# Optimization experiments

Measured on AMD Instinct MI355X. Metric: run time of the kernel, lower is better.

## Reference

```python
import jax, jax.numpy as jnp
import numpy as np

B, S, D, H = 4, 2048, 2048, 16
HD = D // H            # 128 head dim
HID = 5632             # SwiGLU hidden: multiple_of*ceil((2/3*4*D)/multiple_of)
EPS = 1e-6


def setup_inputs() -> dict:
    key = jax.random.key(0)
    ks = jax.random.split(key, 12)
    s = 0.02
    x = jax.random.normal(ks[0], (B, S, D), dtype=jnp.float32)
    # RoPE freqs (theta=10000), complex freqs_cis represented as cos/sin
    inv_freq = 1.0 / (10000.0 ** (np.arange(0, HD, 2, dtype=np.float32) / HD))
    t = np.arange(S, dtype=np.float32)
    ang = np.outer(t, inv_freq)                      # [S, HD/2]
    freqs_cos = jnp.asarray(np.cos(ang), dtype=jnp.float32)
    freqs_sin = jnp.asarray(np.sin(ang), dtype=jnp.float32)
    # additive causal mask [1,1,S,S]
    mask = jnp.where(jnp.triu(jnp.ones((S, S), dtype=bool), k=1), -jnp.inf, 0.0)
    mask = mask.astype(jnp.float32)[None, None]
    return {
        "x": x,
        "freqs_cos": freqs_cos,
        "freqs_sin": freqs_sin,
        "mask": mask,
        "wq": jax.random.normal(ks[1], (D, D), jnp.float32) * s,
        "wk": jax.random.normal(ks[2], (D, D), jnp.float32) * s,
        "wv": jax.random.normal(ks[3], (D, D), jnp.float32) * s,
        "wo": jax.random.normal(ks[4], (D, D), jnp.float32) * s,
        "w1": jax.random.normal(ks[5], (HID, D), jnp.float32) * s,
        "w2": jax.random.normal(ks[6], (D, HID), jnp.float32) * s,
        "w3": jax.random.normal(ks[7], (HID, D), jnp.float32) * s,
        "attn_norm_w": jnp.ones((D,), jnp.float32),
        "ffn_norm_w": jnp.ones((D,), jnp.float32),
        "start_pos": 0,
    }


def rmsnorm(x, w, eps=EPS):
    xf = x.astype(jnp.float32)
    y = xf * jax.lax.rsqrt(jnp.mean(xf * xf, axis=-1, keepdims=True) + eps)
    return y.astype(x.dtype) * w


def apply_rope(q, k, cos, sin):
    # q,k: [B,S,H,HD]; cos,sin: [S,HD/2]
    def rot(x):
        xf = x.astype(jnp.float32).reshape(*x.shape[:-1], HD // 2, 2)
        xr, xi = xf[..., 0], xf[..., 1]
        c = cos[None, :, None, :]
        s = sin[None, :, None, :]
        out = jnp.stack([xr * c - xi * s, xr * s + xi * c], axis=-1)
        return out.reshape(*x.shape).astype(x.dtype)
    return rot(q), rot(k)


def reference(x, freqs_cos, freqs_sin, mask, wq, wk, wv, wo, w1, w2, w3,
              attn_norm_w, ffn_norm_w, start_pos):
    # ---- attention ----
    xa = rmsnorm(x, attn_norm_w)
    q = (xa @ wq.T).reshape(B, S, H, HD)
    k = (xa @ wk.T).reshape(B, S, H, HD)
    v = (xa @ wv.T).reshape(B, S, H, HD)
    q, k = apply_rope(q, k, freqs_cos, freqs_sin)
    # [B,H,S,S] scores (naive, materialized as in original)
    scores = jnp.einsum('bqhd,bkhd->bhqk', q, k) / jnp.sqrt(jnp.float32(HD))
    scores = scores + mask
    attn = jax.nn.softmax(scores, axis=-1)
    o = jnp.einsum('bhqk,bkhd->bqhd', attn, v).reshape(B, S, D)
    h = x + o @ wo.T
    # ---- SwiGLU FFN ----
    hf = rmsnorm(h, ffn_norm_w)
    ff = (jax.nn.silu(hf @ w1.T) * (hf @ w3.T)) @ w2.T
    return h + ff
```

## Files before the change

kernel.cpp:

```cpp
#include <hip/hip_runtime.h>
#include <hip/hip_bf16.h>
#include <stdint.h>

typedef short  bf16x8_t __attribute__((ext_vector_type(8)));
typedef short  bf16x4_t __attribute__((ext_vector_type(4)));
typedef float  f32x4_t  __attribute__((ext_vector_type(4)));
typedef unsigned short u16;
typedef unsigned int   u32;

#define DEV __device__ __forceinline__

DEV u16 f2bf(float f){
  u32 u = __float_as_uint(f);
  u += 0x7fffu + ((u >> 16) & 1u);
  return (u16)(u >> 16);
}
DEV float bf2f(u16 h){ return __uint_as_float(((u32)h) << 16); }

DEV void gl16(const void* g, void* l){
  __builtin_amdgcn_global_load_lds(
      (const __attribute__((address_space(1))) void*)g,
      (__attribute__((address_space(3))) void*)l, 16, 0, 0);
}

#define BAR() __builtin_amdgcn_s_barrier()
#define WL8() asm volatile("s_waitcnt lgkmcnt(8)" ::: "memory")
#define WL0() asm volatile("s_waitcnt lgkmcnt(0)" ::: "memory")

__global__ __launch_bounds__(256) void cvt_k(const float* __restrict__ in,
                                             u16* __restrict__ out, int n8){
  int i = blockIdx.x * 256 + threadIdx.x;
  if (i >= n8) return;
  const float4* p = (const float4*)in;
  float4 a = p[(size_t)i*2], b = p[(size_t)i*2+1];
  bf16x8_t o;
  o[0]=(short)f2bf(a.x); o[1]=(short)f2bf(a.y); o[2]=(short)f2bf(a.z); o[3]=(short)f2bf(a.w);
  o[4]=(short)f2bf(b.x); o[5]=(short)f2bf(b.y); o[6]=(short)f2bf(b.z); o[7]=(short)f2bf(b.w);
  *(bf16x8_t*)(out + (size_t)i*8) = o;
}

__global__ __launch_bounds__(256) void rmsnorm_k(const float* __restrict__ x,
                                                 const float* __restrict__ w,
                                                 u16* __restrict__ y){
  int row = blockIdx.x, t = threadIdx.x;
  const float4* xr = (const float4*)(x + (size_t)row*2048);
  float4 a = xr[t*2], b = xr[t*2+1];
  float ss = a.x*a.x+a.y*a.y+a.z*a.z+a.w*a.w + b.x*b.x+b.y*b.y+b.z*b.z+b.w*b.w;
  #pragma unroll
  for (int m = 32; m; m >>= 1) ss += __shfl_xor(ss, m, 64);
  __shared__ float red[4];
  if ((t & 63) == 0) red[t >> 6] = ss;
  __syncthreads();
  float tot = red[0]+red[1]+red[2]+red[3];
  float rs = rsqrtf(tot * (1.0f/2048.0f) + 1e-6f);
  const float4* wr = (const float4*)w;
  float4 wa = wr[t*2], wb = wr[t*2+1];
  bf16x8_t o;
  o[0]=(short)f2bf(a.x*rs*wa.x); o[1]=(short)f2bf(a.y*rs*wa.y);
  o[2]=(short)f2bf(a.z*rs*wa.z); o[3]=(short)f2bf(a.w*rs*wa.w);
  o[4]=(short)f2bf(b.x*rs*wb.x); o[5]=(short)f2bf(b.y*rs*wb.y);
  o[6]=(short)f2bf(b.z*rs*wb.z); o[7]=(short)f2bf(b.w*rs*wb.w);
  *(bf16x8_t*)(y + (size_t)row*2048 + t*8) = o;
}

__global__ __launch_bounds__(256) void rmsnorm2_k(const float* __restrict__ x,
                                                  const u16* __restrict__ t1,
                                                  const float* __restrict__ w,
                                                  u16* __restrict__ y){
  int row = blockIdx.x, t = threadIdx.x;
  const float4* xr = (const float4*)(x + (size_t)row*2048);
  float4 a = xr[t*2], b = xr[t*2+1];
  bf16x8_t tv = *(const bf16x8_t*)(t1 + (size_t)row*2048 + t*8);
  float h[8];
  h[0]=a.x+bf2f((u16)tv[0]); h[1]=a.y+bf2f((u16)tv[1]);
  h[2]=a.z+bf2f((u16)tv[2]); h[3]=a.w+bf2f((u16)tv[3]);
  h[4]=b.x+bf2f((u16)tv[4]); h[5]=b.y+bf2f((u16)tv[5]);
  h[6]=b.z+bf2f((u16)tv[6]); h[7]=b.w+bf2f((u16)tv[7]);
  float ss = 0.f;
  #pragma unroll
  for (int j=0;j<8;j++) ss += h[j]*h[j];
  #pragma unroll
  for (int m = 32; m; m >>= 1) ss += __shfl_xor(ss, m, 64);
  __shared__ float red[4];
  if ((t & 63) == 0) red[t >> 6] = ss;
  __syncthreads();
  float tot = red[0]+red[1]+red[2]+red[3];
  float rs = rsqrtf(tot * (1.0f/2048.0f) + 1e-6f);
  const float4* wr = (const float4*)w;
  float4 wa = wr[t*2], wb = wr[t*2+1];
  bf16x8_t o;
  o[0]=(short)f2bf(h[0]*rs*wa.x); o[1]=(short)f2bf(h[1]*rs*wa.y);
  o[2]=(short)f2bf(h[2]*rs*wa.z); o[3]=(short)f2bf(h[3]*rs*wa.w);
  o[4]=(short)f2bf(h[4]*rs*wb.x); o[5]=(short)f2bf(h[5]*rs*wb.y);
  o[6]=(short)f2bf(h[6]*rs*wb.z); o[7]=(short)f2bf(h[7]*rs*wb.w);
  *(bf16x8_t*)(y + (size_t)row*2048 + t*8) = o;
}

__global__ __launch_bounds__(256) void rope_k(u16* __restrict__ q, u16* __restrict__ k,
                                              const float* __restrict__ fc,
                                              const float* __restrict__ fs){
  int i = blockIdx.x * 256 + threadIdx.x;
  int ii = i & 63; int h = (i >> 6) & 15; int bs = i >> 10;
  int s = bs & 2047;
  size_t off = (size_t)bs*2048 + h*128 + 2*ii;
  float c = fc[s*64+ii], sn = fs[s*64+ii];
  u32 qq = *(u32*)(q + off);
  float xr = bf2f((u16)(qq & 0xffff)), xi = bf2f((u16)(qq >> 16));
  *(u32*)(q + off) = (u32)f2bf(xr*c - xi*sn) | ((u32)f2bf(xr*sn + xi*c) << 16);
  u32 kk = *(u32*)(k + off);
  xr = bf2f((u16)(kk & 0xffff)); xi = bf2f((u16)(kk >> 16));
  *(u32*)(k + off) = (u32)f2bf(xr*c - xi*sn) | ((u32)f2bf(xr*sn + xi*c) << 16);
}

__global__ __launch_bounds__(256) void transpose_k(const u16* __restrict__ in,
                                                   u16* __restrict__ out){
  __shared__ u16 tile[64*68];
  int tid = threadIdx.x;
  int tm = blockIdx.x >> 5, tn = blockIdx.x & 31;
  const u16* src = in + (size_t)(tm*64)*2048 + tn*64;
  #pragma unroll
  for (int i=0;i<2;i++){
    int idx = i*256 + tid;
    int r = idx >> 3, c8 = (idx & 7)*8;
    *(bf16x8_t*)&tile[r*68 + c8] = *(const bf16x8_t*)(src + (size_t)r*2048 + c8);
  }
  __syncthreads();
  u16* dst = out + (size_t)(tn*64)*8192 + tm*64;
  #pragma unroll
  for (int i=0;i<2;i++){
    int idx = i*256 + tid;
    int oc = idx >> 3, r8 = (idx & 7)*8;
    bf16x8_t v;
    #pragma unroll
    for (int j=0;j<8;j++) v[j] = tile[(r8+j)*68 + oc];
    *(bf16x8_t*)(dst + (size_t)oc*8192 + r8) = v;
  }
}


#define RA(BUF,MH) { \
  Ar[0][0]=*(const bf16x8_t*)(pA +BUF*16384+MH*4096);      \
  Ar[0][1]=*(const bf16x8_t*)(pAx+BUF*16384+MH*4096);      \
  Ar[1][0]=*(const bf16x8_t*)(pA +BUF*16384+MH*4096+1024); \
  Ar[1][1]=*(const bf16x8_t*)(pAx+BUF*16384+MH*4096+1024); \
  Ar[2][0]=*(const bf16x8_t*)(pA +BUF*16384+MH*4096+2048); \
  Ar[2][1]=*(const bf16x8_t*)(pAx+BUF*16384+MH*4096+2048); \
  Ar[3][0]=*(const bf16x8_t*)(pA +BUF*16384+MH*4096+3072); \
  Ar[3][1]=*(const bf16x8_t*)(pAx+BUF*16384+MH*4096+3072); }
#define RB(DST,BUF,NHL) { \
  DST[0][0]=*(const bf16x8_t*)(pB +BUF*16384+NHL*2048);      \
  DST[0][1]=*(const bf16x8_t*)(pBx+BUF*16384+NHL*2048);      \
  DST[1][0]=*(const bf16x8_t*)(pB +BUF*16384+NHL*2048+1024); \
  DST[1][1]=*(const bf16x8_t*)(pBx+BUF*16384+NHL*2048+1024); }
#define STG_A(BUF,HALF,COL) { \
  gl16(gA + (COL) + HALF*K128,       dA + BUF*16384 + HALF*8192); \
  gl16(gA + (COL) + HALF*K128 + K64, dA + BUF*16384 + HALF*8192 + 4096); }
#define STG_B(BUF,HALF,COL) { \
  gl16(gB + (COL) + HALF*K128,       dB + BUF*16384 + HALF*8192); \
  gl16(gB + (COL) + HALF*K128 + K64, dB + BUF*16384 + HALF*8192 + 4096); }

DEV void MMQ(bf16x8_t (&a)[4][2], bf16x8_t (&b)[2][2], int mh, int nhl,
             f32x4_t (&acc)[8][4]){
  __builtin_amdgcn_s_setprio(1);
  #pragma unroll
  for (int kk=0;kk<2;kk++)
    #pragma unroll
    for (int mi=0;mi<4;mi++)
      #pragma unroll
      for (int nj=0;nj<2;nj++)
        acc[mh*4+mi][nhl*2+nj] = __builtin_amdgcn_mfma_f32_16x16x32_bf16(
            a[mi][kk], b[nj][kk], acc[mh*4+mi][nhl*2+nj], 0,0,0);
  __builtin_amdgcn_s_setprio(0);
}

template<int EPI>
__global__ __launch_bounds__(512, 2) void gemm_bt(const u16* __restrict__ A,
                                                  const u16* __restrict__ B,
                                                  void* __restrict__ C,
                                                  const void* __restrict__ aux,
                                                  const void* __restrict__ aux2,
                                                  int M, int N, int K){
  __shared__ __align__(16) u16 sA[2][2][8192];
  __shared__ __align__(16) u16 sB[2][2][8192];
  int tid = threadIdx.x, lane = tid & 63, wave = tid >> 6;
  int l15 = lane & 15, l4 = lane >> 4;
  int nbn = N / 256;
  int nwg = gridDim.x, bid = blockIdx.x;
  int qq = nwg >> 3, rr = nwg & 7;
  int xc = bid & 7, yy = bid >> 3;
  int wg = (xc < rr ? xc*(qq+1) : rr*(qq+1) + (xc-rr)*qq) + yy;
  int tm = wg / nbn, tn = wg % nbn;
  size_t m0 = (size_t)tm*256, n0 = (size_t)tn*256;
  const u16* Ag = A + m0*K;
  const u16* Bg = B + n0*K;
  int wm = wave >> 2, wn = wave & 3;
  int bh = wn >> 1, wn1 = wn & 1;

  int ch0 = l4 ^ (l15 & 7);
  const u16* pA  = &sA[0][wm][l15*64 + ch0*8];
  const u16* pAx = &sA[0][wm][l15*64 + (ch0^4)*8];
  const u16* pB  = &sB[0][bh][(wn1*64 + l15)*64 + ch0*8];
  const u16* pBx = &sB[0][bh][(wn1*64 + l15)*64 + (ch0^4)*8];
  int r0 = tid >> 3;
  int lg = (tid & 7) ^ (r0 & 7);
  const u16* gA = Ag + (size_t)r0*K + lg*8;
  const u16* gB = Bg + (size_t)r0*K + lg*8;
  size_t K64 = (size_t)K*64, K128 = K64*2;
  u16* dA = &sA[0][0][tid*8];
  u16* dB = &sB[0][0][tid*8];

  f32x4_t acc[8][4];
  #pragma unroll
  for (int i=0;i<8;i++)
    #pragma unroll
    for (int j=0;j<4;j++)
      acc[i][j] = (f32x4_t){0.f,0.f,0.f,0.f};
  bf16x8_t Ar[4][2], Br0[2][2], Br1[2][2];
  int nk = K / 64;

  STG_A(0,0,0); STG_A(0,1,0);
  STG_B(0,0,0); STG_B(0,1,0);
  STG_B(1,0,(size_t)64); STG_B(1,1,(size_t)64);
  asm volatile("s_waitcnt vmcnt(4)" ::: "memory");
  BAR();

  for (int i=0; i<nk/2; ++i){
    int T0 = 2*i;
    bool s2 = (T0+2 < nk), s3 = (T0+3 < nk);
    size_t c1 = (size_t)(T0+1)*64, c2 = (size_t)(T0+2)*64, c3 = (size_t)(T0+3)*64;
    RA(0,0); RB(Br0,0,0);
    STG_A(1,0,c1);
    WL8(); BAR(); WL0();
    MMQ(Ar, Br0, 0, 0, acc);
    BAR();
    RB(Br1,0,1);
    STG_A(1,1,c1);
    BAR(); WL0();
    MMQ(Ar, Br1, 0, 1, acc);
    BAR();
    RA(0,1);
    if (s2) STG_B(0,0,c2);
    BAR(); WL0();
    MMQ(Ar, Br0, 1, 0, acc);
    BAR();
    if (s2){
      STG_B(0,1,c2);
      asm volatile("s_waitcnt vmcnt(4)" ::: "memory");
    } else {
      asm volatile("s_waitcnt vmcnt(0)" ::: "memory");
    }
    BAR(); WL0();
    MMQ(Ar, Br1, 1, 1, acc);
    BAR();
    RA(1,0); RB(Br0,1,0);
    if (s2) STG_A(0,0,c2);
    WL8(); BAR(); WL0();
    MMQ(Ar, Br0, 0, 0, acc);
    BAR();
    RB(Br1,1,1);
    if (s2) STG_A(0,1,c2);
    BAR(); WL0();
    MMQ(Ar, Br1, 0, 1, acc);
    BAR();
    RA(1,1);
    if (s3) STG_B(1,0,c3);
    BAR(); WL0();
    MMQ(Ar, Br0, 1, 0, acc);
    BAR();
    if (s3){
      STG_B(1,1,c3);
      asm volatile("s_waitcnt vmcnt(4)" ::: "memory");
    } else {
      asm volatile("s_waitcnt vmcnt(0)" ::: "memory");
    }
    BAR(); WL0();
    MMQ(Ar, Br1, 1, 1, acc);
    BAR();
  }

  #pragma unroll
  for (int am=0; am<8; am++)
    #pragma unroll
    for (int ni=0; ni<4; ni++)
      #pragma unroll
      for (int r=0; r<4; r++){
        float v = acc[am][ni][r];
        size_t rowg = m0 + (am&3)*16 + (am>>2)*64 + wm*128 + l4*4 + r;
        size_t colg = n0 + wn*64 + ni*16 + l15;
        size_t idx = rowg * (size_t)N + colg;
        if constexpr (EPI == 0){
          ((u16*)C)[idx] = f2bf(v);
        } else if constexpr (EPI == 1){
          float s = v / (1.0f + __expf(-v));
          ((u16*)C)[idx] = f2bf(s);
        } else if constexpr (EPI == 2){
          float a = bf2f(((const u16*)aux)[idx]);
          ((u16*)C)[idx] = f2bf(v * a);
        } else {
          float a = ((const float*)aux)[idx];
          float b2 = bf2f(((const u16*)aux2)[idx]);
          ((float*)C)[idx] = v + a + b2;
        }
      }
}

__global__ __launch_bounds__(256) void attn_k(const u16* __restrict__ Q,
                                              const u16* __restrict__ K,
                                              const u16* __restrict__ VT,
                                              u16* __restrict__ O){
  __shared__ __align__(16) u16 sK[32*128];
  __shared__ __align__(16) u16 sVT[128*32];
  int tid = threadIdx.x, lane = tid & 63, wave = tid >> 6;
  int bid = blockIdx.x;
  int qt = 31 - (bid >> 6);
  int bh = bid & 63; int b = bh >> 4, h = bh & 15;
  int l15 = lane & 15, l4 = lane >> 4;
  size_t base = ((size_t)b*2048)*2048 + (size_t)h*128;
  const u16* VTg0 = VT + ((size_t)h*128)*8192 + (size_t)b*2048;
  int qr0 = qt*64 + wave*16;
  int qrow = qr0 + l15;
  bf16x8_t qf[4];
  #pragma unroll
  for (int s=0;s<4;s++)
    qf[s] = *(const bf16x8_t*)(Q + base + (size_t)qrow*2048 + s*32 + l4*8);

  f32x4_t oaccT[8];
  #pragma unroll
  for (int f=0;f<8;f++) oaccT[f] = (f32x4_t){0.f,0.f,0.f,0.f};
  float lrun = 0.f;

  const float cl2 = 0.08838834764831845f * 1.4426950408889634f;
  int nkt = (qt + 1) * 2;
  for (int kt=0; kt<nkt; ++kt){
    __syncthreads();
    const u16* Kg = K + base + (size_t)kt*32*2048;
    #pragma unroll
    for (int i=0;i<2;i++){
      int c = i*256 + tid; int row = c>>4;
      gl16(Kg + (size_t)row*2048 + (size_t)(((c&15) ^ (row&7))*8), &sK[c*8]);
    }
    #pragma unroll
    for (int i=0;i<2;i++){
      int c = i*256 + tid; int d = c>>2;
      gl16(VTg0 + (size_t)d*8192 + kt*32 + (size_t)((((c&3) ^ ((d>>1)&3)))*8),
           &sVT[c*8]);
    }
    __syncthreads();

    if (kt*32 <= qr0 + 15){
      f32x4_t sacc[2];
      sacc[0] = (f32x4_t){0.f,0.f,0.f,0.f};
      sacc[1] = (f32x4_t){0.f,0.f,0.f,0.f};
      __builtin_amdgcn_s_setprio(1);
      #pragma unroll
      for (int n=0;n<2;n++)
        #pragma unroll
        for (int s=0;s<4;s++){
          bf16x8_t kf = *(const bf16x8_t*)
              &sK[(n*16 + l15)*128 + (((s*4 + l4) ^ (l15 & 7))*8)];
          sacc[n] = __builtin_amdgcn_mfma_f32_16x16x32_bf16(kf, qf[s], sacc[n], 0,0,0);
        }
      __builtin_amdgcn_s_setprio(0);
      float sum = 0.f;
      bf16x8_t pa;
      bool diag = (kt*32 + 31 > qr0);
      if (diag){
        #pragma unroll
        for (int j=0;j<8;j++){
          int n = j>>2, r = j&3;
          float p = exp2f(sacc[n][r] * cl2);
          int kg = kt*32 + n*16 + l4*4 + r;
          if (kg > qrow) p = 0.f;
          sum += p;
          pa[j] = (short)f2bf(p);
        }
      } else {
        #pragma unroll
        for (int j=0;j<8;j++){
          float p = exp2f(sacc[j>>2][j&3] * cl2);
          sum += p;
          pa[j] = (short)f2bf(p);
        }
      }
      sum += __shfl_xor(sum, 16, 64);
      sum += __shfl_xor(sum, 32, 64);
      lrun += sum;
      __builtin_amdgcn_s_setprio(1);
      #pragma unroll
      for (int f=0;f<8;f++){
        int d = f*16 + l15;
        bf16x4_t lo = *(const bf16x4_t*)&sVT[d*32 + (((0*4 + l4) ^ (d & 6))*4)];
        bf16x4_t hi = *(const bf16x4_t*)&sVT[d*32 + (((1*4 + l4) ^ (d & 6))*4)];
        bf16x8_t va;
        va[0]=lo[0]; va[1]=lo[1]; va[2]=lo[2]; va[3]=lo[3];
        va[4]=hi[0]; va[5]=hi[1]; va[6]=hi[2]; va[7]=hi[3];
        oaccT[f] = __builtin_amdgcn_mfma_f32_16x16x32_bf16(va, pa, oaccT[f], 0,0,0);
      }
      __builtin_amdgcn_s_setprio(0);
    }
  }
  float inv = 1.0f / lrun;
  size_t orow = (size_t)b*2048 + qrow;
  #pragma unroll
  for (int f=0;f<8;f++){
    bf16x4_t ov;
    ov[0]=(short)f2bf(oaccT[f][0]*inv); ov[1]=(short)f2bf(oaccT[f][1]*inv);
    ov[2]=(short)f2bf(oaccT[f][2]*inv); ov[3]=(short)f2bf(oaccT[f][3]*inv);
    *(bf16x4_t*)(O + orow*2048 + h*128 + f*16 + l4*4) = ov;
  }
}

extern "C" void kernel_launch(void* const* d_in, const int* in_sizes, int n_in,
                              void* d_out, int out_size, void* d_ws, size_t ws_size,
                              hipStream_t stream){
  (void)in_sizes; (void)n_in; (void)out_size; (void)ws_size;
  const float* x   = (const float*)d_in[0];
  const float* fc  = (const float*)d_in[1];
  const float* fs  = (const float*)d_in[2];
  const float* wq  = (const float*)d_in[4];
  const float* wk  = (const float*)d_in[5];
  const float* wv  = (const float*)d_in[6];
  const float* wo  = (const float*)d_in[7];
  const float* w1  = (const float*)d_in[8];
  const float* w2  = (const float*)d_in[9];
  const float* w3  = (const float*)d_in[10];
  const float* anw = (const float*)d_in[11];
  const float* fnw = (const float*)d_in[12];
  float* out = (float*)d_out;
  char* ws = (char*)d_ws;

  const int M = 8192, D = 2048, HID = 5632;
  const size_t WB   = 23068672ull;
  const size_t ACT2 = 33554432ull;

  u16* wbuf = (u16*)(ws);
  u16* xa   = (u16*)(ws + WB);
  u16* qb   = (u16*)(ws + WB + ACT2);
  u16* kb   = (u16*)(ws + WB + 2*ACT2);
  u16* vb   = (u16*)(ws + WB + 3*ACT2);
  u16* g1   = (u16*)(ws + WB + 4*ACT2);
  u16* vt = g1;
  u16* t1 = qb;
  u16* hf = kb;

  rmsnorm_k<<<M, 256, 0, stream>>>(x, anw, xa);

  cvt_k<<<D*D/8/256, 256, 0, stream>>>(wq, wbuf, D*D/8);
  gemm_bt<0><<<(M/256)*(D/256), 512, 0, stream>>>(xa, wbuf, qb, nullptr, nullptr, M, D, D);
  cvt_k<<<D*D/8/256, 256, 0, stream>>>(wk, wbuf, D*D/8);
  gemm_bt<0><<<(M/256)*(D/256), 512, 0, stream>>>(xa, wbuf, kb, nullptr, nullptr, M, D, D);
  cvt_k<<<D*D/8/256, 256, 0, stream>>>(wv, wbuf, D*D/8);
  gemm_bt<0><<<(M/256)*(D/256), 512, 0, stream>>>(xa, wbuf, vb, nullptr, nullptr, M, D, D);

  rope_k<<<32768, 256, 0, stream>>>(qb, kb, fc, fs);
  transpose_k<<<4096, 256, 0, stream>>>(vb, vt);

  attn_k<<<2048, 256, 0, stream>>>(qb, kb, vt, xa);

  cvt_k<<<D*D/8/256, 256, 0, stream>>>(wo, wbuf, D*D/8);
  gemm_bt<0><<<(M/256)*(D/256), 512, 0, stream>>>(xa, wbuf, t1, nullptr, nullptr, M, D, D);

  rmsnorm2_k<<<M, 256, 0, stream>>>(x, t1, fnw, hf);

  cvt_k<<<HID*D/8/256, 256, 0, stream>>>(w1, wbuf, HID*D/8);
  gemm_bt<1><<<(M/256)*(HID/256), 512, 0, stream>>>(hf, wbuf, g1, nullptr, nullptr, M, HID, D);
  cvt_k<<<HID*D/8/256, 256, 0, stream>>>(w3, wbuf, HID*D/8);
  gemm_bt<2><<<(M/256)*(HID/256), 512, 0, stream>>>(hf, wbuf, g1, g1, nullptr, M, HID, D);
  cvt_k<<<HID*D/8/256, 256, 0, stream>>>(w2, wbuf, HID*D/8);
  gemm_bt<4><<<(M/256)*(D/256), 512, 0, stream>>>(g1, wbuf, out, x, t1, M, D, HID);
}
```

Measured before the change: 1.117 ms.

## Fuse QKV GEMMs, vectorize GEMM epilogue, double-buffer attention K/V loads

Converts wq, wk and wv into one contiguous weight buffer and runs a single N=6144 GEMM whose epilogue routes each column block to the q, k or v output. This removes two GEMM launches and their tail effects. The MFMA operand order is swapped so each lane holds four consecutive columns, which lets every epilogue write (and read aux data) as vectors of 4 instead of scalar strided stores. The attention kernel gets double-buffered LDS for K and V^T, so the next tile is prefetched while the current one is computed. This doubles the attention kernel's LDS use and enlarges the weight workspace.

```diff
diff --git a/kernel.cpp b/kernel.cpp
--- a/kernel.cpp
+++ b/kernel.cpp
@@ -169,7 +169,7 @@
       #pragma unroll
       for (int nj=0;nj<2;nj++)
         acc[mh*4+mi][nhl*2+nj] = __builtin_amdgcn_mfma_f32_16x16x32_bf16(
-            a[mi][kk], b[nj][kk], acc[mh*4+mi][nhl*2+nj], 0,0,0);
+            b[nj][kk], a[mi][kk], acc[mh*4+mi][nhl*2+nj], 0,0,0);
   __builtin_amdgcn_s_setprio(0);
 }
 
@@ -279,37 +279,53 @@
   }
 
   #pragma unroll
-  for (int am=0; am<8; am++)
-    #pragma unroll
-    for (int ni=0; ni<4; ni++)
-      #pragma unroll
-      for (int r=0; r<4; r++){
-        float v = acc[am][ni][r];
-        size_t rowg = m0 + (am&3)*16 + (am>>2)*64 + wm*128 + l4*4 + r;
-        size_t colg = n0 + wn*64 + ni*16 + l15;
-        size_t idx = rowg * (size_t)N + colg;
-        if constexpr (EPI == 0){
-          ((u16*)C)[idx] = f2bf(v);
-        } else if constexpr (EPI == 1){
-          float s = v / (1.0f + __expf(-v));
-          ((u16*)C)[idx] = f2bf(s);
-        } else if constexpr (EPI == 2){
-          float a = bf2f(((const u16*)aux)[idx]);
-          ((u16*)C)[idx] = f2bf(v * a);
-        } else {
-          float a = ((const float*)aux)[idx];
-          float b2 = bf2f(((const u16*)aux2)[idx]);
-          ((float*)C)[idx] = v + a + b2;
-        }
+  for (int am=0; am<8; am++){
+    size_t m = m0 + (am&3)*16 + (am>>2)*64 + wm*128 + l15;
+    #pragma unroll
+    for (int ni=0; ni<4; ni++){
+      size_t nb = n0 + wn*64 + ni*16 + l4*4;
+      f32x4_t v = acc[am][ni];
+      if constexpr (EPI == 0){
+        bf16x4_t o;
+        #pragma unroll
+        for (int r=0;r<4;r++) o[r]=(short)f2bf(v[r]);
+        *(bf16x4_t*)((u16*)C + m*(size_t)N + nb) = o;
+      } else if constexpr (EPI == 1){
+        bf16x4_t o;
+        #pragma unroll
+        for (int r=0;r<4;r++){ float s=v[r]/(1.0f+__expf(-v[r])); o[r]=(short)f2bf(s); }
+        *(bf16x4_t*)((u16*)C + m*(size_t)N + nb) = o;
+      } else if constexpr (EPI == 2){
+        bf16x4_t a = *(const bf16x4_t*)((const u16*)aux + m*(size_t)N + nb);
+        bf16x4_t o;
+        #pragma unroll
+        for (int r=0;r<4;r++) o[r]=(short)f2bf(v[r]*bf2f((u16)a[r]));
+        *(bf16x4_t*)((u16*)C + m*(size_t)N + nb) = o;
+      } else if constexpr (EPI == 4){
+        float4 xv = *(const float4*)((const float*)aux + m*(size_t)N + nb);
+        bf16x4_t tv = *(const bf16x4_t*)((const u16*)aux2 + m*(size_t)N + nb);
+        float4 o;
+        o.x = v[0]+xv.x+bf2f((u16)tv[0]); o.y = v[1]+xv.y+bf2f((u16)tv[1]);
+        o.z = v[2]+xv.z+bf2f((u16)tv[2]); o.w = v[3]+xv.w+bf2f((u16)tv[3]);
+        *(float4*)((float*)C + m*(size_t)N + nb) = o;
+      } else {
+        int mat = (int)(nb >> 11);
+        u16* dst = (mat==0) ? (u16*)C : (mat==1) ? (u16*)aux : (u16*)aux2;
+        bf16x4_t o;
+        #pragma unroll
+        for (int r=0;r<4;r++) o[r]=(short)f2bf(v[r]);
+        *(bf16x4_t*)(dst + m*2048 + (nb & 2047)) = o;
       }
+    }
+  }
 }
 
 __global__ __launch_bounds__(256) void attn_k(const u16* __restrict__ Q,
                                               const u16* __restrict__ K,
                                               const u16* __restrict__ VT,
                                               u16* __restrict__ O){
-  __shared__ __align__(16) u16 sK[32*128];
-  __shared__ __align__(16) u16 sVT[128*32];
+  __shared__ __align__(16) u16 sK[2][32*128];
+  __shared__ __align__(16) u16 sVT[2][128*32];
   int tid = threadIdx.x, lane = tid & 63, wave = tid >> 6;
   int bid = blockIdx.x;
   int qt = 31 - (bid >> 6);
@@ -331,22 +347,30 @@
 
   const float cl2 = 0.08838834764831845f * 1.4426950408889634f;
   int nkt = (qt + 1) * 2;
-  for (int kt=0; kt<nkt; ++kt){
-    __syncthreads();
-    const u16* Kg = K + base + (size_t)kt*32*2048;
+
+  auto STG = [&](int t, int buf){
+    const u16* Kg = K + base + (size_t)t*32*2048;
     #pragma unroll
     for (int i=0;i<2;i++){
       int c = i*256 + tid; int row = c>>4;
-      gl16(Kg + (size_t)row*2048 + (size_t)(((c&15) ^ (row&7))*8), &sK[c*8]);
+      gl16(Kg + (size_t)row*2048 + (size_t)(((c&15) ^ (row&7))*8), &sK[buf][c*8]);
     }
     #pragma unroll
     for (int i=0;i<2;i++){
       int c = i*256 + tid; int d = c>>2;
-      gl16(VTg0 + (size_t)d*8192 + kt*32 + (size_t)((((c&3) ^ ((d>>1)&3)))*8),
-           &sVT[c*8]);
-    }
-    __syncthreads();
-
+      gl16(VTg0 + (size_t)d*8192 + t*32 + (size_t)((((c&3) ^ ((d>>1)&3)))*8),
+           &sVT[buf][c*8]);
+    }
+  };
+
+  STG(0, 0);
+  STG(1, 1);
+
+  for (int kt=0; kt<nkt; ++kt){
+    if (kt < nkt-1) asm volatile("s_waitcnt vmcnt(4)" ::: "memory");
+    else            asm volatile("s_waitcnt vmcnt(0)" ::: "memory");
+    BAR();
+    int buf = kt & 1;
     if (kt*32 <= qr0 + 15){
       f32x4_t sacc[2];
       sacc[0] = (f32x4_t){0.f,0.f,0.f,0.f};
@@ -357,7 +381,7 @@
         #pragma unroll
         for (int s=0;s<4;s++){
           bf16x8_t kf = *(const bf16x8_t*)
-              &sK[(n*16 + l15)*128 + (((s*4 + l4) ^ (l15 & 7))*8)];
+              &sK[buf][(n*16 + l15)*128 + (((s*4 + l4) ^ (l15 & 7))*8)];
           sacc[n] = __builtin_amdgcn_mfma_f32_16x16x32_bf16(kf, qf[s], sacc[n], 0,0,0);
         }
       __builtin_amdgcn_s_setprio(0);
@@ -389,8 +413,8 @@
       #pragma unroll
       for (int f=0;f<8;f++){
         int d = f*16 + l15;
-        bf16x4_t lo = *(const bf16x4_t*)&sVT[d*32 + (((0*4 + l4) ^ (d & 6))*4)];
-        bf16x4_t hi = *(const bf16x4_t*)&sVT[d*32 + (((1*4 + l4) ^ (d & 6))*4)];
+        bf16x4_t lo = *(const bf16x4_t*)&sVT[buf][d*32 + (((0*4 + l4) ^ (d & 6))*4)];
+        bf16x4_t hi = *(const bf16x4_t*)&sVT[buf][d*32 + (((1*4 + l4) ^ (d & 6))*4)];
         bf16x8_t va;
         va[0]=lo[0]; va[1]=lo[1]; va[2]=lo[2]; va[3]=lo[3];
         va[4]=hi[0]; va[5]=hi[1]; va[6]=hi[2]; va[7]=hi[3];
@@ -398,6 +422,8 @@
       }
       __builtin_amdgcn_s_setprio(0);
     }
+    BAR();
+    if (kt+2 < nkt) STG(kt+2, buf);
   }
   float inv = 1.0f / lrun;
   size_t orow = (size_t)b*2048 + qrow;
@@ -430,7 +456,7 @@
   char* ws = (char*)d_ws;
 
   const int M = 8192, D = 2048, HID = 5632;
-  const size_t WB   = 23068672ull;
+  const size_t WB   = 25165824ull;
   const size_t ACT2 = 33554432ull;
 
   u16* wbuf = (u16*)(ws);
@@ -445,12 +471,10 @@
 
   rmsnorm_k<<<M, 256, 0, stream>>>(x, anw, xa);
 
-  cvt_k<<<D*D/8/256, 256, 0, stream>>>(wq, wbuf, D*D/8);
-  gemm_bt<0><<<(M/256)*(D/256), 512, 0, stream>>>(xa, wbuf, qb, nullptr, nullptr, M, D, D);
-  cvt_k<<<D*D/8/256, 256, 0, stream>>>(wk, wbuf, D*D/8);
-  gemm_bt<0><<<(M/256)*(D/256), 512, 0, stream>>>(xa, wbuf, kb, nullptr, nullptr, M, D, D);
-  cvt_k<<<D*D/8/256, 256, 0, stream>>>(wv, wbuf, D*D/8);
-  gemm_bt<0><<<(M/256)*(D/256), 512, 0, stream>>>(xa, wbuf, vb, nullptr, nullptr, M, D, D);
+  cvt_k<<<D*D/8/256, 256, 0, stream>>>(wq, wbuf,            D*D/8);
+  cvt_k<<<D*D/8/256, 256, 0, stream>>>(wk, wbuf +   D*D,    D*D/8);
+  cvt_k<<<D*D/8/256, 256, 0, stream>>>(wv, wbuf + 2*D*D,    D*D/8);
+  gemm_bt<6><<<(M/256)*(6144/256), 512, 0, stream>>>(xa, wbuf, qb, kb, vb, M, 6144, D);
 
   rope_k<<<32768, 256, 0, stream>>>(qb, kb, fc, fs);
   transpose_k<<<4096, 256, 0, stream>>>(vb, vt);
```

New measurement: 1.138 ms. No clear change (+1.9%).
